# Kernel tuning notes

Hardware: AMD Instinct MI355X
Metric: run time of the kernel (lower is better)

The kernel has to match this reference:

```python
import jax, jax.numpy as jnp
import numpy as np

T, D, E, K = 16384, 4096, 64, 2


def setup_inputs() -> dict:
    key = jax.random.key(0)
    k1, k2, k3 = jax.random.split(key, 3)
    x = jax.random.normal(k1, (T, D), dtype=jnp.float32)
    # torch nn.Linear default init scale ~ 1/sqrt(fan_in)
    gate_w = jax.random.normal(k2, (E, D), dtype=jnp.float32) * (1.0 / np.sqrt(D))
    gate_b = jax.random.normal(k3, (E,), dtype=jnp.float32) * (1.0 / np.sqrt(D))
    return {"x": x, "gate_w": gate_w, "gate_b": gate_b}


def reference(x, gate_w, gate_b):
    # gate linear: [T, D] @ [D, E] + [E] -> [T, E]
    router_logits = jnp.einsum("td,ed->te", x, gate_w) + gate_b
    # softmax over experts in float32 (matches F.softmax(..., dtype=torch.float))
    router_probs = jax.nn.softmax(router_logits.astype(jnp.float32), axis=-1)
    # top-k experts per token
    router_weights, select_expert_indices = jax.lax.top_k(router_probs, K)  # [T, K]
    # renormalize selected weights to sum to 1
    router_weights = router_weights / jnp.sum(router_weights, axis=-1, keepdims=True)
    router_weights = router_weights.astype(x.dtype)
    # one-hot mask [T, K, E] -> permute(2,1,0) -> [E, K, T]
    expert_mask = jax.nn.one_hot(select_expert_indices, E, dtype=jnp.int32)
    expert_mask = jnp.transpose(expert_mask, (2, 1, 0))
    return (router_logits, router_weights, select_expert_indices, expert_mask)
```

## Files before the change

kernel.cpp:

```cpp
#include <hip/hip_runtime.h>
#include <math.h>

#define T_TOK 16384
#define D_DIM 4096
#define E_EXP 64

#define OFF_W   (T_TOK * E_EXP)
#define OFF_I   (OFF_W + T_TOK * 2)
#define OFF_M   (OFF_I + T_TOK * 2)

__global__ __launch_bounds__(256, 1) void gemm_kernel(
    const float* __restrict__ x, const float* __restrict__ w,
    const float* __restrict__ b, float* __restrict__ logits) {
  __shared__ float lds[16384];

  const int tid  = threadIdx.x;
  const int tok0 = blockIdx.x * 64;
  const int wave = tid >> 6;
  const int lane = tid & 63;
  const int a    = lane >> 3;
  const int bg   = lane & 7;
  const int srow = lane >> 3;
  const int sf   = lane & 7;

  float acc[8][8];
#pragma unroll
  for (int i = 0; i < 8; i++)
#pragma unroll
    for (int j = 0; j < 8; j++) acc[i][j] = 0.f;

  float* xs = lds + wave * 2048;
  float* wsm = lds + 8192 + wave * 2048;

  for (int c = 0; c < 32; c++) {
    const int dbase = wave * 1024 + c * 32;
    __syncthreads();
#pragma unroll
    for (int i = 0; i < 8; i++) {
      const int row = i * 8 + srow;
      const float4 xv = *(const float4*)(x + (size_t)(tok0 + row) * D_DIM + dbase + sf * 4);
      xs[(sf * 4 + 0) * 64 + row] = xv.x;
      xs[(sf * 4 + 1) * 64 + row] = xv.y;
      xs[(sf * 4 + 2) * 64 + row] = xv.z;
      xs[(sf * 4 + 3) * 64 + row] = xv.w;
      const float4 wv = *(const float4*)(w + (size_t)row * D_DIM + dbase + sf * 4);
      wsm[(sf * 4 + 0) * 64 + row] = wv.x;
      wsm[(sf * 4 + 1) * 64 + row] = wv.y;
      wsm[(sf * 4 + 2) * 64 + row] = wv.z;
      wsm[(sf * 4 + 3) * 64 + row] = wv.w;
    }
    __syncthreads();
#pragma unroll
    for (int dd = 0; dd < 32; dd++) {
      const float4 xv0 = *(const float4*)(xs + dd * 64 + a * 8);
      const float4 xv1 = *(const float4*)(xs + dd * 64 + a * 8 + 4);
      const float4 wv0 = *(const float4*)(wsm + dd * 64 + bg * 8);
      const float4 wv1 = *(const float4*)(wsm + dd * 64 + bg * 8 + 4);
      const float xr[8] = {xv0.x, xv0.y, xv0.z, xv0.w, xv1.x, xv1.y, xv1.z, xv1.w};
      const float wr[8] = {wv0.x, wv0.y, wv0.z, wv0.w, wv1.x, wv1.y, wv1.z, wv1.w};
#pragma unroll
      for (int i = 0; i < 8; i++)
#pragma unroll
        for (int j = 0; j < 8; j++) acc[i][j] = fmaf(xr[i], wr[j], acc[i][j]);
    }
  }

  __syncthreads();
#pragma unroll
  for (int i = 0; i < 8; i++) {
    const int tok = a * 8 + i;
    float* dst = lds + wave * 4096 + tok * 64 + bg * 8;
    *(float4*)(dst)     = make_float4(acc[i][0], acc[i][1], acc[i][2], acc[i][3]);
    *(float4*)(dst + 4) = make_float4(acc[i][4], acc[i][5], acc[i][6], acc[i][7]);
  }
  __syncthreads();
#pragma unroll
  for (int v = 0; v < 4; v++) {
    const int f = v * 1024 + tid * 4;
    const float4 s0 = *(const float4*)(lds + f);
    const float4 s1 = *(const float4*)(lds + 4096 + f);
    const float4 s2 = *(const float4*)(lds + 8192 + f);
    const float4 s3 = *(const float4*)(lds + 12288 + f);
    const int e = f & 63;
    const float4 bb = *(const float4*)(b + e);
    float4 o;
    o.x = s0.x + s1.x + s2.x + s3.x + bb.x;
    o.y = s0.y + s1.y + s2.y + s3.y + bb.y;
    o.z = s0.z + s1.z + s2.z + s3.z + bb.z;
    o.w = s0.w + s1.w + s2.w + s3.w + bb.w;
    *(float4*)(logits + (size_t)(tok0 + (f >> 6)) * E_EXP + e) = o;
  }
}

__global__ __launch_bounds__(256) void router_kernel(
    const float* __restrict__ logits, float* __restrict__ out) {
  const int t = blockIdx.x * 256 + threadIdx.x;
  const float* lp = logits + (size_t)t * E_EXP;

  float l[64];
#pragma unroll
  for (int i = 0; i < 64; i += 4) {
    const float4 v = *(const float4*)(lp + i);
    l[i] = v.x; l[i + 1] = v.y; l[i + 2] = v.z; l[i + 3] = v.w;
  }
  float m = l[0];
#pragma unroll
  for (int i = 1; i < 64; i++) m = fmaxf(m, l[i]);
  float e[64];
  float s = 0.f;
#pragma unroll
  for (int i = 0; i < 64; i++) { e[i] = expf(l[i] - m); s += e[i]; }

  float v1 = -1.f, v2 = -1.f;
  int i1 = 0, i2 = 0;
#pragma unroll
  for (int i = 0; i < 64; i++) {
    const float ei = e[i];
    if (ei > v1) { v2 = v1; i2 = i1; v1 = ei; i1 = i; }
    else if (ei > v2) { v2 = ei; i2 = i; }
  }
  const float pr1 = v1 / s, pr2 = v2 / s;
  const float rs = pr1 + pr2;
  out[OFF_W + t * 2 + 0] = pr1 / rs;
  out[OFF_W + t * 2 + 1] = pr2 / rs;
  out[OFF_I + t * 2 + 0] = (float)i1;
  out[OFF_I + t * 2 + 1] = (float)i2;
  out[OFF_M + (size_t)(i1 * 2 + 0) * T_TOK + t] = 1.0f;
  out[OFF_M + (size_t)(i2 * 2 + 1) * T_TOK + t] = 1.0f;
}

extern "C" void kernel_launch(void* const* d_in, const int* in_sizes, int n_in,
                              void* d_out, int out_size, void* d_ws, size_t ws_size,
                              hipStream_t stream) {
  const float* x  = (const float*)d_in[0];
  const float* w  = (const float*)d_in[1];
  const float* b  = (const float*)d_in[2];
  float* out = (float*)d_out;

  hipMemsetAsync(out + OFF_M, 0, (size_t)E_EXP * 2 * T_TOK * sizeof(float), stream);

  gemm_kernel<<<T_TOK / 64, 256, 0, stream>>>(x, w, b, out);
  router_kernel<<<T_TOK / 256, 256, 0, stream>>>(out, out);
}
```

Measured before the change: 468.5 us.

## Fuse router into GEMM with register-prefetched pipeline and smaller token tiles

Merges the logits GEMM and the softmax/top-2 router into one kernel, removing the second launch and the logits round trip. Token tiles shrink to 32 per block with two blocks per CU, and each wave prefetches the next chunk into registers while computing on padded per-wave LDS, so the in-loop block barriers are gone. Top-2 weights are computed directly from the logit difference instead of a full softmax. In exchange, the gate weights are reloaded by twice as many blocks, and the router runs on only 32 threads per block.

Measured after the change: 412.3 us. 12.0% less time.

```diff
diff --git a/kernel.cpp b/kernel.cpp
--- a/kernel.cpp
+++ b/kernel.cpp
@@ -9,136 +9,166 @@
 #define OFF_I   (OFF_W + T_TOK * 2)
 #define OFF_M   (OFF_I + T_TOK * 2)
 
-__global__ __launch_bounds__(256, 1) void gemm_kernel(
+#define XS_STRIDE 36
+#define WS_STRIDE 68
+#define XS_SIZE   (32 * XS_STRIDE)
+#define WS_SIZE   (32 * WS_STRIDE)
+#define WAVE_LDS  (XS_SIZE + WS_SIZE)
+#define RED_STRIDE 68
+#define LG_BASE   (4 * WAVE_LDS)
+#define LDS_FLOATS (LG_BASE + 32 * RED_STRIDE)
+
+__global__ __launch_bounds__(256, 2) void moe_router_kernel(
     const float* __restrict__ x, const float* __restrict__ w,
-    const float* __restrict__ b, float* __restrict__ logits) {
-  __shared__ float lds[16384];
+    const float* __restrict__ b, float* __restrict__ out) {
+  __shared__ __align__(16) float lds[LDS_FLOATS];
 
   const int tid  = threadIdx.x;
-  const int tok0 = blockIdx.x * 64;
   const int wave = tid >> 6;
   const int lane = tid & 63;
-  const int a    = lane >> 3;
-  const int bg   = lane & 7;
-  const int srow = lane >> 3;
-  const int sf   = lane & 7;
+  const int tok0 = blockIdx.x * 32;
+  const int q = lane & 7;
+  const int r = lane >> 3;
+  const int tg = lane >> 3;
+  const int eg = lane & 7;
 
-  float acc[8][8];
+  float* xs  = lds + wave * WAVE_LDS;
+  float* wsb = xs + XS_SIZE;
+
+  float acc[4][8];
 #pragma unroll
-  for (int i = 0; i < 8; i++)
+  for (int i = 0; i < 4; i++)
 #pragma unroll
     for (int j = 0; j < 8; j++) acc[i][j] = 0.f;
 
-  float* xs = lds + wave * 2048;
-  float* wsm = lds + 8192 + wave * 2048;
+  const float* xbase = x + (size_t)tok0 * D_DIM + wave * 1024 + q * 4;
+  const float* wbase = w + wave * 1024 + q * 4;
 
-  for (int c = 0; c < 32; c++) {
-    const int dbase = wave * 1024 + c * 32;
-    __syncthreads();
+  auto load_chunk = [&](int c, float4* xv, float4* wv) {
+    const float* xp = xbase + c * 32;
 #pragma unroll
-    for (int i = 0; i < 8; i++) {
-      const int row = i * 8 + srow;
-      const float4 xv = *(const float4*)(x + (size_t)(tok0 + row) * D_DIM + dbase + sf * 4);
-      xs[(sf * 4 + 0) * 64 + row] = xv.x;
-      xs[(sf * 4 + 1) * 64 + row] = xv.y;
-      xs[(sf * 4 + 2) * 64 + row] = xv.z;
-      xs[(sf * 4 + 3) * 64 + row] = xv.w;
-      const float4 wv = *(const float4*)(w + (size_t)row * D_DIM + dbase + sf * 4);
-      wsm[(sf * 4 + 0) * 64 + row] = wv.x;
-      wsm[(sf * 4 + 1) * 64 + row] = wv.y;
-      wsm[(sf * 4 + 2) * 64 + row] = wv.z;
-      wsm[(sf * 4 + 3) * 64 + row] = wv.w;
+    for (int p = 0; p < 4; p++)
+      xv[p] = *(const float4*)(xp + (size_t)(p * 8 + r) * D_DIM);
+    const float* wp = wbase + c * 32;
+#pragma unroll
+    for (int p = 0; p < 8; p++)
+      wv[p] = *(const float4*)(wp + (size_t)(p * 8 + r) * D_DIM);
+  };
+  auto stage_chunk = [&](const float4* xv, const float4* wv) {
+#pragma unroll
+    for (int p = 0; p < 4; p++) {
+      const int row = p * 8 + r;
+      xs[(q * 4 + 0) * XS_STRIDE + row] = xv[p].x;
+      xs[(q * 4 + 1) * XS_STRIDE + row] = xv[p].y;
+      xs[(q * 4 + 2) * XS_STRIDE + row] = xv[p].z;
+      xs[(q * 4 + 3) * XS_STRIDE + row] = xv[p].w;
     }
-    __syncthreads();
 #pragma unroll
+    for (int p = 0; p < 8; p++) {
+      const int e = p * 8 + r;
+      wsb[(q * 4 + 0) * WS_STRIDE + e] = wv[p].x;
+      wsb[(q * 4 + 1) * WS_STRIDE + e] = wv[p].y;
+      wsb[(q * 4 + 2) * WS_STRIDE + e] = wv[p].z;
+      wsb[(q * 4 + 3) * WS_STRIDE + e] = wv[p].w;
+    }
+  };
+  auto compute_chunk = [&]() {
+#pragma unroll 8
     for (int dd = 0; dd < 32; dd++) {
-      const float4 xv0 = *(const float4*)(xs + dd * 64 + a * 8);
-      const float4 xv1 = *(const float4*)(xs + dd * 64 + a * 8 + 4);
-      const float4 wv0 = *(const float4*)(wsm + dd * 64 + bg * 8);
-      const float4 wv1 = *(const float4*)(wsm + dd * 64 + bg * 8 + 4);
-      const float xr[8] = {xv0.x, xv0.y, xv0.z, xv0.w, xv1.x, xv1.y, xv1.z, xv1.w};
-      const float wr[8] = {wv0.x, wv0.y, wv0.z, wv0.w, wv1.x, wv1.y, wv1.z, wv1.w};
+      const float4 xr = *(const float4*)(xs + dd * XS_STRIDE + tg * 4);
+      const float4 w0 = *(const float4*)(wsb + dd * WS_STRIDE + eg * 8);
+      const float4 w1 = *(const float4*)(wsb + dd * WS_STRIDE + eg * 8 + 4);
+      const float xa[4] = {xr.x, xr.y, xr.z, xr.w};
+      const float wa[8] = {w0.x, w0.y, w0.z, w0.w, w1.x, w1.y, w1.z, w1.w};
 #pragma unroll
-      for (int i = 0; i < 8; i++)
+      for (int i = 0; i < 4; i++)
 #pragma unroll
-        for (int j = 0; j < 8; j++) acc[i][j] = fmaf(xr[i], wr[j], acc[i][j]);
+        for (int j = 0; j < 8; j++) acc[i][j] = fmaf(xa[i], wa[j], acc[i][j]);
+    }
+  };
+
+  float4 xv0[4], wv0[8], xv1[4], wv1[8];
+  load_chunk(0, xv0, wv0);
+#pragma unroll 1
+  for (int c = 0; c < 32; c += 2) {
+    stage_chunk(xv0, wv0);
+    load_chunk(c + 1, xv1, wv1);
+    compute_chunk();
+    stage_chunk(xv1, wv1);
+    if (c + 2 < 32) load_chunk(c + 2, xv0, wv0);
+    compute_chunk();
+  }
+
+  {
+    float* red = xs;
+#pragma unroll
+    for (int i = 0; i < 4; i++) {
+      const int row = tg * 4 + i;
+      float* rp = red + row * RED_STRIDE + eg * 8;
+      *(float4*)rp       = make_float4(acc[i][0], acc[i][1], acc[i][2], acc[i][3]);
+      *(float4*)(rp + 4) = make_float4(acc[i][4], acc[i][5], acc[i][6], acc[i][7]);
     }
   }
+  __syncthreads();
 
-  __syncthreads();
+  {
+    const int tok = tid >> 3;
+    const int e8  = (tid & 7) * 8;
+    float4 s0 = make_float4(0.f, 0.f, 0.f, 0.f);
+    float4 s1 = make_float4(0.f, 0.f, 0.f, 0.f);
 #pragma unroll
-  for (int i = 0; i < 8; i++) {
-    const int tok = a * 8 + i;
-    float* dst = lds + wave * 4096 + tok * 64 + bg * 8;
-    *(float4*)(dst)     = make_float4(acc[i][0], acc[i][1], acc[i][2], acc[i][3]);
-    *(float4*)(dst + 4) = make_float4(acc[i][4], acc[i][5], acc[i][6], acc[i][7]);
+    for (int wv = 0; wv < 4; wv++) {
+      const float* rp = lds + wv * WAVE_LDS + tok * RED_STRIDE + e8;
+      const float4 a0 = *(const float4*)rp;
+      const float4 a1 = *(const float4*)(rp + 4);
+      s0.x += a0.x; s0.y += a0.y; s0.z += a0.z; s0.w += a0.w;
+      s1.x += a1.x; s1.y += a1.y; s1.z += a1.z; s1.w += a1.w;
+    }
+    const float4 b0 = *(const float4*)(b + e8);
+    const float4 b1 = *(const float4*)(b + e8 + 4);
+    s0.x += b0.x; s0.y += b0.y; s0.z += b0.z; s0.w += b0.w;
+    s1.x += b1.x; s1.y += b1.y; s1.z += b1.z; s1.w += b1.w;
+    float* lp = out + (size_t)(tok0 + tok) * E_EXP + e8;
+    *(float4*)lp       = s0;
+    *(float4*)(lp + 4) = s1;
+    float* lg = lds + LG_BASE + tok * RED_STRIDE + e8;
+    *(float4*)lg       = s0;
+    *(float4*)(lg + 4) = s1;
   }
   __syncthreads();
-#pragma unroll
-  for (int v = 0; v < 4; v++) {
-    const int f = v * 1024 + tid * 4;
-    const float4 s0 = *(const float4*)(lds + f);
-    const float4 s1 = *(const float4*)(lds + 4096 + f);
-    const float4 s2 = *(const float4*)(lds + 8192 + f);
-    const float4 s3 = *(const float4*)(lds + 12288 + f);
-    const int e = f & 63;
-    const float4 bb = *(const float4*)(b + e);
-    float4 o;
-    o.x = s0.x + s1.x + s2.x + s3.x + bb.x;
-    o.y = s0.y + s1.y + s2.y + s3.y + bb.y;
-    o.z = s0.z + s1.z + s2.z + s3.z + bb.z;
-    o.w = s0.w + s1.w + s2.w + s3.w + bb.w;
-    *(float4*)(logits + (size_t)(tok0 + (f >> 6)) * E_EXP + e) = o;
+
+  if (tid < 32) {
+    const int tok = tid;
+    const float* lg = lds + LG_BASE + tok * RED_STRIDE;
+    float v1 = -1e30f, v2 = -1e30f;
+    int i1 = 0, i2 = 0;
+    for (int e = 0; e < 64; e++) {
+      const float le = lg[e];
+      if (le > v1)      { v2 = v1; i2 = i1; v1 = le; i1 = e; }
+      else if (le > v2) { v2 = le; i2 = e; }
+    }
+    const float d  = expf(v2 - v1);
+    const float w1 = 1.f / (1.f + d);
+    const float w2 = d * w1;
+    const int t = tok0 + tok;
+    out[OFF_W + t * 2 + 0] = w1;
+    out[OFF_W + t * 2 + 1] = w2;
+    out[OFF_I + t * 2 + 0] = (float)i1;
+    out[OFF_I + t * 2 + 1] = (float)i2;
+    out[OFF_M + (size_t)(i1 * 2 + 0) * T_TOK + t] = 1.0f;
+    out[OFF_M + (size_t)(i2 * 2 + 1) * T_TOK + t] = 1.0f;
   }
-}
-
-__global__ __launch_bounds__(256) void router_kernel(
-    const float* __restrict__ logits, float* __restrict__ out) {
-  const int t = blockIdx.x * 256 + threadIdx.x;
-  const float* lp = logits + (size_t)t * E_EXP;
-
-  float l[64];
-#pragma unroll
-  for (int i = 0; i < 64; i += 4) {
-    const float4 v = *(const float4*)(lp + i);
-    l[i] = v.x; l[i + 1] = v.y; l[i + 2] = v.z; l[i + 3] = v.w;
-  }
-  float m = l[0];
-#pragma unroll
-  for (int i = 1; i < 64; i++) m = fmaxf(m, l[i]);
-  float e[64];
-  float s = 0.f;
-#pragma unroll
-  for (int i = 0; i < 64; i++) { e[i] = expf(l[i] - m); s += e[i]; }
-
-  float v1 = -1.f, v2 = -1.f;
-  int i1 = 0, i2 = 0;
-#pragma unroll
-  for (int i = 0; i < 64; i++) {
-    const float ei = e[i];
-    if (ei > v1) { v2 = v1; i2 = i1; v1 = ei; i1 = i; }
-    else if (ei > v2) { v2 = ei; i2 = i; }
-  }
-  const float pr1 = v1 / s, pr2 = v2 / s;
-  const float rs = pr1 + pr2;
-  out[OFF_W + t * 2 + 0] = pr1 / rs;
-  out[OFF_W + t * 2 + 1] = pr2 / rs;
-  out[OFF_I + t * 2 + 0] = (float)i1;
-  out[OFF_I + t * 2 + 1] = (float)i2;
-  out[OFF_M + (size_t)(i1 * 2 + 0) * T_TOK + t] = 1.0f;
-  out[OFF_M + (size_t)(i2 * 2 + 1) * T_TOK + t] = 1.0f;
 }
 
 extern "C" void kernel_launch(void* const* d_in, const int* in_sizes, int n_in,
                               void* d_out, int out_size, void* d_ws, size_t ws_size,
                               hipStream_t stream) {
-  const float* x  = (const float*)d_in[0];
-  const float* w  = (const float*)d_in[1];
-  const float* b  = (const float*)d_in[2];
+  const float* x = (const float*)d_in[0];
+  const float* w = (const float*)d_in[1];
+  const float* b = (const float*)d_in[2];
   float* out = (float*)d_out;
 
   hipMemsetAsync(out + OFF_M, 0, (size_t)E_EXP * 2 * T_TOK * sizeof(float), stream);
 
-  gemm_kernel<<<T_TOK / 64, 256, 0, stream>>>(x, w, b, out);
-  router_kernel<<<T_TOK / 256, 256, 0, stream>>>(out, out);
+  moe_router_kernel<<<T_TOK / 32, 256, 0, stream>>>(x, w, b, out);
 }
```

## Replace FP32 FMA GEMM with split-fp16 MFMA kernel fused with router top-k

Applied to the files above, without the earlier changes.

Replaces the scalar FP32 FMA GEMM with a matrix-core kernel using fp16 MFMA on a hi/lo split of x and the weights (three products) to keep near-fp32 accuracy. The weights are converted and pre-laid-out by a new prep kernel, and x chunks are double-buffered in LDS with register prefetch. Softmax, top-2 and one-hot writes are fused into the GEMM epilogue with wave shuffles, and the renormalised weights are computed from the logit difference, which removes the second kernel and its reread of the logits. The split-precision scheme adds conversion work per x element and may change accuracy slightly.

New measurement: 437.1 us. 1.07x faster.

```diff
diff --git a/kernel.cpp b/kernel.cpp
--- a/kernel.cpp
+++ b/kernel.cpp
@@ -9,136 +9,203 @@
 #define OFF_I   (OFF_W + T_TOK * 2)
 #define OFF_M   (OFF_I + T_TOK * 2)
 
-__global__ __launch_bounds__(256, 1) void gemm_kernel(
-    const float* __restrict__ x, const float* __restrict__ w,
-    const float* __restrict__ b, float* __restrict__ logits) {
-  __shared__ float lds[16384];
+#define NCHUNK    64
+#define CH_HALVES 4096
+
+typedef _Float16 half8 __attribute__((ext_vector_type(8)));
+typedef float    f32x4 __attribute__((ext_vector_type(4)));
+
+__global__ __launch_bounds__(256) void prep_w(const float* __restrict__ w,
+                                              _Float16* __restrict__ ws_hi,
+                                              _Float16* __restrict__ ws_lo) {
+  const int g   = blockIdx.x * 256 + threadIdx.x;
+  const int exp = g >> 8;
+  const int kb  = (g & 255) * 16;
+  const float* src = w + (size_t)exp * D_DIM + kb;
+  float vals[16];
+#pragma unroll
+  for (int i = 0; i < 4; i++) {
+    const float4 f = *(const float4*)(src + i * 4);
+    vals[i * 4 + 0] = f.x; vals[i * 4 + 1] = f.y;
+    vals[i * 4 + 2] = f.z; vals[i * 4 + 3] = f.w;
+  }
+  const int n_tile = exp >> 4, nn = exp & 15;
+#pragma unroll
+  for (int part = 0; part < 2; part++) {
+    const int k0 = kb + part * 8;
+    const int c = k0 >> 6, rem = k0 & 63;
+    const int s = rem >> 5, q = (rem >> 3) & 3;
+    const size_t off = (size_t)c * CH_HALVES + (n_tile * 2 + s) * 512 + (nn + 16 * q) * 8;
+    half8 hv, lv;
+#pragma unroll
+    for (int j = 0; j < 8; j++) {
+      const float xf = vals[part * 8 + j];
+      const _Float16 h = (_Float16)xf;
+      hv[j] = h;
+      lv[j] = (_Float16)((xf - (float)h) * 2048.0f);
+    }
+    *(half8*)(ws_hi + off) = hv;
+    *(half8*)(ws_lo + off) = lv;
+  }
+}
+
+__global__ __launch_bounds__(256, 1) void moe_mfma(
+    const float* __restrict__ x, const _Float16* __restrict__ ws_hi,
+    const _Float16* __restrict__ ws_lo, const float* __restrict__ bias,
+    float* __restrict__ out) {
+  __shared__ __align__(16) _Float16 smem[2][4][CH_HALVES];
 
   const int tid  = threadIdx.x;
-  const int tok0 = blockIdx.x * 64;
   const int wave = tid >> 6;
   const int lane = tid & 63;
-  const int a    = lane >> 3;
-  const int bg   = lane & 7;
-  const int srow = lane >> 3;
-  const int sf   = lane & 7;
-
-  float acc[8][8];
-#pragma unroll
-  for (int i = 0; i < 8; i++)
-#pragma unroll
-    for (int j = 0; j < 8; j++) acc[i][j] = 0.f;
-
-  float* xs = lds + wave * 2048;
-  float* wsm = lds + 8192 + wave * 2048;
-
-  for (int c = 0; c < 32; c++) {
-    const int dbase = wave * 1024 + c * 32;
+  const int tok0 = blockIdx.x * 64;
+  const int stok = tid >> 2;
+  const int so4  = tid & 3;
+
+  f32x4 accm[4], accc[4];
+#pragma unroll
+  for (int t = 0; t < 4; t++) {
+    accm[t] = (f32x4){0.f, 0.f, 0.f, 0.f};
+    accc[t] = (f32x4){0.f, 0.f, 0.f, 0.f};
+  }
+
+  float4 xr[2][4];
+  uint4  br[2][4];
+
+  auto loadx = [&](int c, float4* xv) {
+    const float* p = x + (size_t)(tok0 + stok) * D_DIM + c * 64 + so4 * 8;
+    xv[0] = ((const float4*)p)[0];
+    xv[1] = ((const float4*)p)[1];
+    xv[2] = ((const float4*)(p + 32))[0];
+    xv[3] = ((const float4*)(p + 32))[1];
+  };
+  auto loadB = [&](int c, uint4* bv) {
+    const uint4* ph = (const uint4*)(ws_hi + (size_t)c * CH_HALVES) + tid * 2;
+    bv[0] = ph[0]; bv[1] = ph[1];
+    const uint4* pl = (const uint4*)(ws_lo + (size_t)c * CH_HALVES) + tid * 2;
+    bv[2] = pl[0]; bv[3] = pl[1];
+  };
+  auto stage = [&](int buf, const float4* xv, const uint4* bv) {
+    const int g = stok >> 4, m = stok & 15;
+#pragma unroll
+    for (int p = 0; p < 2; p++) {
+      const int o = so4 + 4 * p;
+      const int s = o >> 2, q = o & 3;
+      const int off = (g * 2 + s) * 512 + (m + 16 * q) * 8;
+      const float4 f0 = xv[2 * p], f1 = xv[2 * p + 1];
+      const float vv[8] = {f0.x, f0.y, f0.z, f0.w, f1.x, f1.y, f1.z, f1.w};
+      half8 hv, lv;
+#pragma unroll
+      for (int j = 0; j < 8; j++) {
+        const _Float16 h = (_Float16)vv[j];
+        hv[j] = h;
+        lv[j] = (_Float16)((vv[j] - (float)h) * 2048.0f);
+      }
+      *(half8*)(&smem[buf][0][off]) = hv;
+      *(half8*)(&smem[buf][1][off]) = lv;
+    }
+    *(uint4*)(&smem[buf][2][tid * 16])     = bv[0];
+    *(uint4*)(&smem[buf][2][tid * 16 + 8]) = bv[1];
+    *(uint4*)(&smem[buf][3][tid * 16])     = bv[2];
+    *(uint4*)(&smem[buf][3][tid * 16 + 8]) = bv[3];
+  };
+  auto compute = [&](int buf) {
+#pragma unroll
+    for (int s = 0; s < 2; s++) {
+      const half8 ah = *(const half8*)(&smem[buf][0][(wave * 2 + s) * 512 + lane * 8]);
+      const half8 al = *(const half8*)(&smem[buf][1][(wave * 2 + s) * 512 + lane * 8]);
+#pragma unroll
+      for (int t = 0; t < 4; t++) {
+        const half8 bh = *(const half8*)(&smem[buf][2][(t * 2 + s) * 512 + lane * 8]);
+        const half8 bl = *(const half8*)(&smem[buf][3][(t * 2 + s) * 512 + lane * 8]);
+        accm[t] = __builtin_amdgcn_mfma_f32_16x16x32_f16(ah, bh, accm[t], 0, 0, 0);
+        accc[t] = __builtin_amdgcn_mfma_f32_16x16x32_f16(ah, bl, accc[t], 0, 0, 0);
+        accc[t] = __builtin_amdgcn_mfma_f32_16x16x32_f16(al, bh, accc[t], 0, 0, 0);
+      }
+    }
+  };
+
+  loadx(0, xr[0]); loadB(0, br[0]);
+  stage(0, xr[0], br[0]);
+  loadx(1, xr[1]); loadB(1, br[1]);
+  __syncthreads();
+#pragma unroll 1
+  for (int c = 0; c < NCHUNK; c += 2) {
+    if (c + 2 < NCHUNK) { loadx(c + 2, xr[0]); loadB(c + 2, br[0]); }
+    compute(0);
+    stage(1, xr[1], br[1]);
     __syncthreads();
-#pragma unroll
-    for (int i = 0; i < 8; i++) {
-      const int row = i * 8 + srow;
-      const float4 xv = *(const float4*)(x + (size_t)(tok0 + row) * D_DIM + dbase + sf * 4);
-      xs[(sf * 4 + 0) * 64 + row] = xv.x;
-      xs[(sf * 4 + 1) * 64 + row] = xv.y;
-      xs[(sf * 4 + 2) * 64 + row] = xv.z;
-      xs[(sf * 4 + 3) * 64 + row] = xv.w;
-      const float4 wv = *(const float4*)(w + (size_t)row * D_DIM + dbase + sf * 4);
-      wsm[(sf * 4 + 0) * 64 + row] = wv.x;
-      wsm[(sf * 4 + 1) * 64 + row] = wv.y;
-      wsm[(sf * 4 + 2) * 64 + row] = wv.z;
-      wsm[(sf * 4 + 3) * 64 + row] = wv.w;
-    }
+    if (c + 3 < NCHUNK) { loadx(c + 3, xr[1]); loadB(c + 3, br[1]); }
+    compute(1);
+    if (c + 2 < NCHUNK) stage(0, xr[0], br[0]);
     __syncthreads();
-#pragma unroll
-    for (int dd = 0; dd < 32; dd++) {
-      const float4 xv0 = *(const float4*)(xs + dd * 64 + a * 8);
-      const float4 xv1 = *(const float4*)(xs + dd * 64 + a * 8 + 4);
-      const float4 wv0 = *(const float4*)(wsm + dd * 64 + bg * 8);
-      const float4 wv1 = *(const float4*)(wsm + dd * 64 + bg * 8 + 4);
-      const float xr[8] = {xv0.x, xv0.y, xv0.z, xv0.w, xv1.x, xv1.y, xv1.z, xv1.w};
-      const float wr[8] = {wv0.x, wv0.y, wv0.z, wv0.w, wv1.x, wv1.y, wv1.z, wv1.w};
-#pragma unroll
-      for (int i = 0; i < 8; i++)
-#pragma unroll
-        for (int j = 0; j < 8; j++) acc[i][j] = fmaf(xr[i], wr[j], acc[i][j]);
-    }
-  }
-
-  __syncthreads();
-#pragma unroll
-  for (int i = 0; i < 8; i++) {
-    const int tok = a * 8 + i;
-    float* dst = lds + wave * 4096 + tok * 64 + bg * 8;
-    *(float4*)(dst)     = make_float4(acc[i][0], acc[i][1], acc[i][2], acc[i][3]);
-    *(float4*)(dst + 4) = make_float4(acc[i][4], acc[i][5], acc[i][6], acc[i][7]);
-  }
-  __syncthreads();
-#pragma unroll
-  for (int v = 0; v < 4; v++) {
-    const int f = v * 1024 + tid * 4;
-    const float4 s0 = *(const float4*)(lds + f);
-    const float4 s1 = *(const float4*)(lds + 4096 + f);
-    const float4 s2 = *(const float4*)(lds + 8192 + f);
-    const float4 s3 = *(const float4*)(lds + 12288 + f);
-    const int e = f & 63;
-    const float4 bb = *(const float4*)(b + e);
-    float4 o;
-    o.x = s0.x + s1.x + s2.x + s3.x + bb.x;
-    o.y = s0.y + s1.y + s2.y + s3.y + bb.y;
-    o.z = s0.z + s1.z + s2.z + s3.z + bb.z;
-    o.w = s0.w + s1.w + s2.w + s3.w + bb.w;
-    *(float4*)(logits + (size_t)(tok0 + (f >> 6)) * E_EXP + e) = o;
-  }
-}
-
-__global__ __launch_bounds__(256) void router_kernel(
-    const float* __restrict__ logits, float* __restrict__ out) {
-  const int t = blockIdx.x * 256 + threadIdx.x;
-  const float* lp = logits + (size_t)t * E_EXP;
-
-  float l[64];
-#pragma unroll
-  for (int i = 0; i < 64; i += 4) {
-    const float4 v = *(const float4*)(lp + i);
-    l[i] = v.x; l[i + 1] = v.y; l[i + 2] = v.z; l[i + 3] = v.w;
-  }
-  float m = l[0];
-#pragma unroll
-  for (int i = 1; i < 64; i++) m = fmaxf(m, l[i]);
-  float e[64];
-  float s = 0.f;
-#pragma unroll
-  for (int i = 0; i < 64; i++) { e[i] = expf(l[i] - m); s += e[i]; }
-
-  float v1 = -1.f, v2 = -1.f;
-  int i1 = 0, i2 = 0;
-#pragma unroll
-  for (int i = 0; i < 64; i++) {
-    const float ei = e[i];
-    if (ei > v1) { v2 = v1; i2 = i1; v1 = ei; i1 = i; }
-    else if (ei > v2) { v2 = ei; i2 = i; }
-  }
-  const float pr1 = v1 / s, pr2 = v2 / s;
-  const float rs = pr1 + pr2;
-  out[OFF_W + t * 2 + 0] = pr1 / rs;
-  out[OFF_W + t * 2 + 1] = pr2 / rs;
-  out[OFF_I + t * 2 + 0] = (float)i1;
-  out[OFF_I + t * 2 + 1] = (float)i2;
-  out[OFF_M + (size_t)(i1 * 2 + 0) * T_TOK + t] = 1.0f;
-  out[OFF_M + (size_t)(i2 * 2 + 1) * T_TOK + t] = 1.0f;
+  }
+
+  const int cc = lane & 15, q = lane >> 4;
+  float fin[4][4];
+#pragma unroll
+  for (int t = 0; t < 4; t++) {
+    const float bb = bias[t * 16 + cc];
+#pragma unroll
+    for (int r = 0; r < 4; r++)
+      fin[t][r] = accm[t][r] + accc[t][r] * 4.8828125e-4f + bb;
+  }
+#pragma unroll
+  for (int r = 0; r < 4; r++) {
+    const int trow = tok0 + wave * 16 + q * 4 + r;
+#pragma unroll
+    for (int t = 0; t < 4; t++)
+      out[(size_t)trow * E_EXP + t * 16 + cc] = fin[t][r];
+  }
+
+#pragma unroll
+  for (int r = 0; r < 4; r++) {
+    float v1 = fin[0][r]; int i1 = cc;
+    float v2 = -3.4e38f;  int i2 = 0;
+#pragma unroll
+    for (int t = 1; t < 4; t++) {
+      const float vc = fin[t][r]; const int ic = t * 16 + cc;
+      if (vc > v1)      { v2 = v1; i2 = i1; v1 = vc; i1 = ic; }
+      else if (vc > v2) { v2 = vc; i2 = ic; }
+    }
+#pragma unroll
+    for (int mk = 1; mk <= 8; mk <<= 1) {
+      const float ov1 = __shfl_xor(v1, mk); const int oi1 = __shfl_xor(i1, mk);
+      const float ov2 = __shfl_xor(v2, mk); const int oi2 = __shfl_xor(i2, mk);
+      if ((ov1 > v1) || (ov1 == v1 && oi1 < i1)) {
+        const bool s2 = (v1 > ov2) || (v1 == ov2 && i1 < oi2);
+        v2 = s2 ? v1 : ov2; i2 = s2 ? i1 : oi2;
+        v1 = ov1; i1 = oi1;
+      } else {
+        const bool s2 = (ov1 > v2) || (ov1 == v2 && oi1 < i2);
+        v2 = s2 ? ov1 : v2; i2 = s2 ? oi1 : i2;
+      }
+    }
+    if (cc == 0) {
+      const int trow = tok0 + wave * 16 + q * 4 + r;
+      const float d  = expf(v2 - v1);
+      const float w1 = 1.f / (1.f + d);
+      out[OFF_W + trow * 2 + 0] = w1;
+      out[OFF_W + trow * 2 + 1] = d * w1;
+      out[OFF_I + trow * 2 + 0] = (float)i1;
+      out[OFF_I + trow * 2 + 1] = (float)i2;
+      out[OFF_M + (size_t)(i1 * 2 + 0) * T_TOK + trow] = 1.0f;
+      out[OFF_M + (size_t)(i2 * 2 + 1) * T_TOK + trow] = 1.0f;
+    }
+  }
 }
 
 extern "C" void kernel_launch(void* const* d_in, const int* in_sizes, int n_in,
                               void* d_out, int out_size, void* d_ws, size_t ws_size,
                               hipStream_t stream) {
-  const float* x  = (const float*)d_in[0];
-  const float* w  = (const float*)d_in[1];
-  const float* b  = (const float*)d_in[2];
+  const float* x    = (const float*)d_in[0];
+  const float* w    = (const float*)d_in[1];
+  const float* bias = (const float*)d_in[2];
   float* out = (float*)d_out;
+  _Float16* ws_hi = (_Float16*)d_ws;
+  _Float16* ws_lo = ws_hi + (size_t)NCHUNK * CH_HALVES;
 
   hipMemsetAsync(out + OFF_M, 0, (size_t)E_EXP * 2 * T_TOK * sizeof(float), stream);
-
-  gemm_kernel<<<T_TOK / 64, 256, 0, stream>>>(x, w, b, out);
-  router_kernel<<<T_TOK / 256, 256, 0, stream>>>(out, out);
+  prep_w<<<E_EXP * D_DIM / (256 * 16), 256, 0, stream>>>(w, ws_hi, ws_lo);
+  moe_mfma<<<T_TOK / 64, 256, 0, stream>>>(x, ws_hi, ws_lo, bias, out);
 }
```
